# Optimization experiments

Hardware: AMD Instinct MI355X
Metric: run time of the kernel (lower is better)

Reference implementation:

```python
import jax, jax.numpy as jnp
import numpy as np

N_HEADS = 8
N_GROUPS = 32
EPS = 1e-5


def setup_inputs() -> dict:
    key = jax.random.key(0)
    ks = jax.random.split(key, 3)
    B, C, H, W = 16, 512, 32, 32
    x = jax.random.normal(ks[0], (B, C, H, W), dtype=jnp.float32)
    gn_w = jnp.ones((C,), dtype=jnp.float32)
    gn_b = jnp.zeros((C,), dtype=jnp.float32)
    qkv_w = jax.random.normal(ks[1], (3 * C, C), dtype=jnp.float32) * (1.0 / np.sqrt(C))
    qkv_b = jnp.zeros((3 * C,), dtype=jnp.float32)
    proj_w = jax.random.normal(ks[2], (C, C), dtype=jnp.float32) * (1.0 / np.sqrt(C))
    proj_b = jnp.zeros((C,), dtype=jnp.float32)
    return {"x": x, "gn_w": gn_w, "gn_b": gn_b, "qkv_w": qkv_w,
            "qkv_b": qkv_b, "proj_w": proj_w, "proj_b": proj_b}


def reference(x, gn_w, gn_b, qkv_w, qkv_b, proj_w, proj_b):
    b, c, h, w = x.shape
    t = h * w
    xf = x.reshape(b, c, t)                       # [B, C, T]

    # GroupNorm(32, C): normalize over (C//G, T) per group, then per-channel affine
    xg = xf.reshape(b, N_GROUPS, -1)              # [B, G, (C//G)*T]
    mean = xg.mean(axis=-1, keepdims=True)
    var = xg.var(axis=-1, keepdims=True)
    xn = ((xg - mean) * jax.lax.rsqrt(var + EPS)).reshape(b, c, t)
    xn = xn * gn_w[:, None] + gn_b[:, None]

    # 1x1 conv = channel GEMM -> qkv [B, 3C, T]
    qkv = jnp.einsum('oc,bct->bot', qkv_w, xn) + qkv_b[:, None]

    # legacy head split: reshape BEFORE splitting q,k,v
    qkv = qkv.reshape(b * N_HEADS, 3 * c // N_HEADS, t)
    ch = qkv.shape[1] // 3                        # = C // n_heads
    q, k, v = jnp.split(qkv, 3, axis=1)
    scale = 1.0 / np.sqrt(np.sqrt(ch))
    weight = jnp.einsum('bct,bcs->bts', q * scale, k * scale)
    weight = jax.nn.softmax(weight.astype(jnp.float32), axis=-1).astype(weight.dtype)
    a = jnp.einsum('bts,bcs->bct', weight, v)     # [B*H, ch, T]

    hh = a.reshape(b, c, t)
    hh = jnp.einsum('oc,bct->bot', proj_w, hh) + proj_b[:, None]
    return (xf + hh).reshape(b, c, h, w)
```

## Files before the change

kernel.cpp:

```cpp
#include <hip/hip_runtime.h>
#include <hip/hip_bf16.h>
#include <stdint.h>

#define B_ 16
#define C_ 512
#define T_ 1024
#define NH_ 8

typedef __attribute__((ext_vector_type(8))) short bf16x8;
typedef __attribute__((ext_vector_type(4))) float f32x4;
typedef __attribute__((ext_vector_type(16))) float f32x16;
typedef __attribute__((ext_vector_type(4))) unsigned short us4;
typedef __attribute__((ext_vector_type(4))) uint32_t u32x4;
typedef __attribute__((ext_vector_type(2))) uint32_t u32x2;

__device__ __forceinline__ unsigned short f2bf(float f) {
  union { float f; uint32_t u; } v; v.f = f;
  uint32_t r = v.u + 0x7FFFu + ((v.u >> 16) & 1u);
  return (unsigned short)(r >> 16);
}

__device__ __forceinline__ uint32_t cvtpk_bf16(float lo, float hi) {
  uint32_t r;
  asm("v_cvt_pk_bf16_f32 %0, %1, %2" : "=v"(r) : "v"(lo), "v"(hi));
  return r;
}

__device__ __forceinline__ f32x4 mfma_bf16(bf16x8 a, bf16x8 b, f32x4 c) {
  asm("v_mfma_f32_16x16x32_bf16 %0, %1, %2, %0" : "+v"(c) : "v"(a), "v"(b));
  return c;
}

__device__ __forceinline__ f32x16 mfma32_bf16(bf16x8 a, bf16x8 b, f32x16 c) {
  asm("v_mfma_f32_32x32x16_bf16 %0, %1, %2, %0" : "+v"(c) : "v"(a), "v"(b));
  return c;
}

__device__ __forceinline__ void swap32(uint32_t& a, uint32_t& b) {
  asm("v_permlane32_swap_b32 %0, %1" : "+v"(a), "+v"(b));
}

typedef const __attribute__((address_space(1))) uint32_t* gas1_t;
typedef __attribute__((address_space(3))) uint32_t* las3_t;

__device__ __forceinline__ void async16(const void* g, void* lds) {
  __builtin_amdgcn_global_load_lds((gas1_t)(uintptr_t)g,
                                   (las3_t)(uint32_t)(uintptr_t)lds, 16, 0, 0);
}

#define SCLF 0.18033688011112044f

__global__ __launch_bounds__(256) void convert_w_kernel(
    const float* __restrict__ qkv_w, const float* __restrict__ proj_w,
    unsigned short* __restrict__ wq, unsigned short* __restrict__ wp) {
  int i = blockIdx.x * 256 + threadIdx.x;
  const float4* src;
  unsigned short* dst;
  int rel = i;
  if (i < 196608) { src = (const float4*)qkv_w; dst = wq; }
  else            { src = (const float4*)proj_w; dst = wp; rel = i - 196608; }
  float4 v = src[rel];
  us4 o;
  o.x = f2bf(v.x); o.y = f2bf(v.y); o.z = f2bf(v.z); o.w = f2bf(v.w);
  *(us4*)&dst[(size_t)rel * 4] = o;
}

__global__ __launch_bounds__(256) void groupnorm_kernel(
    const float* __restrict__ x, const float* __restrict__ gn_w,
    const float* __restrict__ gn_b, unsigned short* __restrict__ xnT) {
  const int blk = blockIdx.x;
  const int b = blk >> 5, g = blk & 31;
  const int tid = threadIdx.x;
  const float4* x4 = (const float4*)(x + (((size_t)(b * C_ + g * 16)) << 10));

  float4 v[16];
  float s1 = 0.f, s2 = 0.f;
#pragma unroll
  for (int i = 0; i < 16; ++i) {
    v[i] = x4[tid + i * 256];
    s1 += v[i].x + v[i].y + v[i].z + v[i].w;
    s2 += v[i].x * v[i].x + v[i].y * v[i].y + v[i].z * v[i].z + v[i].w * v[i].w;
  }
#pragma unroll
  for (int m = 32; m; m >>= 1) { s1 += __shfl_xor(s1, m); s2 += __shfl_xor(s2, m); }

  __shared__ float r1[4], r2[4], stats[2];
  const int wv = tid >> 6;
  if ((tid & 63) == 0) { r1[wv] = s1; r2[wv] = s2; }
  __syncthreads();
  if (tid == 0) {
    float a = r1[0] + r1[1] + r1[2] + r1[3];
    float q = r2[0] + r2[1] + r2[2] + r2[3];
    float mean = a * (1.f / 16384.f);
    float var = q * (1.f / 16384.f) - mean * mean;
    stats[0] = mean;
    stats[1] = rsqrtf(var + 1e-5f);
  }
  __syncthreads();
  const float mean = stats[0], rsig = stats[1];

  float wc[16], bc[16];
#pragma unroll
  for (int c = 0; c < 16; ++c) {
    const float w0 = gn_w[g * 16 + c] * rsig;
    wc[c] = w0;
    bc[c] = gn_b[g * 16 + c] - mean * w0;
  }
#pragma unroll
  for (int r = 0; r < 4; ++r) {
    uint32_t o[8];
#pragma unroll
    for (int c2 = 0; c2 < 8; ++c2) {
      const float a = ((const float*)&v[2 * c2])[r] * wc[2 * c2] + bc[2 * c2];
      const float q = ((const float*)&v[2 * c2 + 1])[r] * wc[2 * c2 + 1] + bc[2 * c2 + 1];
      o[c2] = cvtpk_bf16(a, q);
    }
    unsigned short* dst = &xnT[(((size_t)(b * T_ + tid * 4 + r)) << 9) + g * 16];
    u32x4 lo; lo.x = o[0]; lo.y = o[1]; lo.z = o[2]; lo.w = o[3];
    u32x4 hi; hi.x = o[4]; hi.y = o[5]; hi.z = o[6]; hi.w = o[7];
    *(u32x4*)dst = lo;
    *(u32x4*)(dst + 8) = hi;
  }
}

template <int MODE>
__global__ __launch_bounds__(256) void gemm_nt_kernel(
    const unsigned short* __restrict__ A, const unsigned short* __restrict__ Bw,
    const float* __restrict__ bias, unsigned short* __restrict__ qfb,
    unsigned short* __restrict__ kfb, unsigned short* __restrict__ vfb,
    const float* __restrict__ xres, float* __restrict__ out) {
  const int b = blockIdx.z;
  const int m0 = blockIdx.y * 128;
  const int n0 = blockIdx.x * 128;
  const int tid = threadIdx.x;
  const int w = tid >> 6, ln = tid & 63;
  const int r15 = ln & 15, r4 = ln >> 4;

  __shared__ __attribute__((aligned(16))) char smem[40960];
  unsigned short* As = (unsigned short*)smem;
  unsigned short* Bs = (unsigned short*)(smem + 16384);

  const unsigned short* Ab = A + (((size_t)(b * T_ + m0)) << 9);
  const unsigned short* Bb = Bw + ((size_t)n0 << 9);

  f32x4 acc[4][4] = {};
  const int wm = (w >> 1) << 6, wn = (w & 1) << 6;

  for (int kt = 0; kt < 8; ++kt) {
    const int k0 = kt << 6;
    __syncthreads();
#pragma unroll
    for (int j = 0; j < 4; ++j) {
      const int slot = (j << 6) + ln;
      const int row = slot >> 3;
      const int chg = (slot & 7) ^ (row & 7);
      async16(Ab + (((size_t)(w * 32 + row)) << 9) + k0 + chg * 8,
              (char*)As + w * 4096 + j * 1024);
      async16(Bb + (((size_t)(w * 32 + row)) << 9) + k0 + chg * 8,
              (char*)Bs + w * 4096 + j * 1024);
    }
    __syncthreads();
#pragma unroll
    for (int kk = 0; kk < 2; ++kk) {
      bf16x8 af[4], bfr[4];
#pragma unroll
      for (int i = 0; i < 4; ++i) {
        const int ra = wm + i * 16 + r15;
        const int ch = r4 + kk * 4;
        af[i] = *(const bf16x8*)((const char*)As + ra * 128 + ((ch ^ (ra & 7)) << 4));
        const int rb = wn + i * 16 + r15;
        bfr[i] = *(const bf16x8*)((const char*)Bs + rb * 128 + ((ch ^ (rb & 7)) << 4));
      }
#pragma unroll
      for (int i = 0; i < 4; ++i)
#pragma unroll
        for (int j = 0; j < 4; ++j)
          acc[i][j] = mfma_bf16(af[i], bfr[j], acc[i][j]);
    }
  }

  if constexpr (MODE == 0) {
    __syncthreads();
    const int seg = w & 1;
    const int typ3 = (n0 >> 7) % 3;
    int st;
    if (typ3 == 0) st = seg;
    else if (typ3 == 1) st = seg ? 0 : 2;
    else st = seg ? 2 : 1;
    const int hseg = (n0 + seg * 64) / 192;
    char* segp = smem + seg * 20480;
    const int q5 = ln & 31, hi = ln >> 5;

    if (st < 2) {
      unsigned short* qkL = (unsigned short*)segp;
      const float scl = (st == 0) ? SCLF : 1.f;
#pragma unroll
      for (int j = 0; j < 4; ++j) {
        const int c = j * 16 + r15;
        const float bsv = bias[n0 + seg * 64 + c];
#pragma unroll
        for (int i = 0; i < 4; ++i) {
          const int t0 = wm + i * 16 + r4 * 4;
#pragma unroll
          for (int r = 0; r < 4; ++r)
            qkL[(t0 + r) * 80 + c] = f2bf((acc[i][j][r] + bsv) * scl);
        }
      }
      __syncthreads();
      unsigned short* dst = (st == 0) ? qfb : kfb;
      const size_t hb = ((size_t)(b * NH_ + hseg)) << 16;
#pragma unroll
      for (int u = 0; u < 8; ++u) {
        const int qbl = (w >> 1) * 2 + (u >> 2);
        const int ks = u & 3;
        bf16x8 val = *(const bf16x8*)&qkL[(qbl * 32 + q5) * 80 + ks * 16 + hi * 8];
        *(bf16x8*)&dst[hb + ((((m0 >> 5) + qbl) * 4 + ks) * 64 + ln) * 8] = val;
      }
    } else {
      unsigned short* vL = (unsigned short*)segp;
#pragma unroll
      for (int j = 0; j < 4; ++j) {
        const int c = j * 16 + r15;
        const float bsv = bias[n0 + seg * 64 + c];
#pragma unroll
        for (int i = 0; i < 4; ++i) {
          const int t0 = wm + i * 16 + r4 * 4;
          u32x2 pk;
          pk.x = cvtpk_bf16(acc[i][j][0] + bsv, acc[i][j][1] + bsv);
          pk.y = cvtpk_bf16(acc[i][j][2] + bsv, acc[i][j][3] + bsv);
          *(u32x2*)&vL[c * 144 + t0] = pk;
        }
      }
      __syncthreads();
      const size_t hb = ((size_t)(b * NH_ + hseg)) << 16;
      const int ktl = w >> 1;
#pragma unroll
      for (int u = 0; u < 8; ++u) {
        const int ks = u >> 1, cb = u & 1;
        bf16x8 val = *(const bf16x8*)&vL[(cb * 32 + q5) * 144 +
                                         ktl * 64 + ks * 16 + hi * 8];
        *(bf16x8*)&vfb[hb + ((((m0 >> 6) + ktl) * 8 + ks * 2 + cb) * 64 + ln) * 8] = val;
      }
    }
  } else {
#pragma unroll
    for (int i = 0; i < 4; ++i) {
      const int t = m0 + wm + i * 16 + r4 * 4;
#pragma unroll
      for (int j = 0; j < 4; ++j) {
        const int o = n0 + wn + j * 16 + r15;
        const float bsv = bias[o];
        const size_t base = (((size_t)(b * C_ + o)) << 10) + t;
        const float4 xr = *(const float4*)&xres[base];
        float4 ov;
        ov.x = acc[i][j][0] + bsv + xr.x;
        ov.y = acc[i][j][1] + bsv + xr.y;
        ov.z = acc[i][j][2] + bsv + xr.z;
        ov.w = acc[i][j][3] + bsv + xr.w;
        *(float4*)&out[base] = ov;
      }
    }
  }
}

__global__ __launch_bounds__(256) void attn_kernel(
    const unsigned short* __restrict__ Qf, const unsigned short* __restrict__ Kf,
    const unsigned short* __restrict__ Vf, unsigned short* __restrict__ aT) {
  const int lin = blockIdx.x;
  const int bh = (lin & 7) * 16 + (lin >> 5);
  const int qt = (lin >> 3) & 3;
  const int b = bh >> 3, h = bh & 7;
  const int tid = threadIdx.x;
  const int w = tid >> 6, ln = tid & 63;
  const int q5 = ln & 31, hi = ln >> 5;

  const unsigned short* qb_ = Qf + ((size_t)bh << 16);
  const unsigned short* kb = Kf + ((size_t)bh << 16);
  const unsigned short* vb = Vf + ((size_t)bh << 16);
  const int qw0 = qt * 8 + w * 2;

  bf16x8 qf[2][4];
#pragma unroll
  for (int qb = 0; qb < 2; ++qb)
#pragma unroll
    for (int ks = 0; ks < 4; ++ks)
      qf[qb][ks] = *(const bf16x8*)(qb_ + ((((qw0 + qb) * 4 + ks) * 64 + ln) << 3));

  float l_run[2] = {0.f, 0.f};
  f32x16 acc[2][2] = {};

  for (int t = 0; t < 16; ++t) {
    bf16x8 kf[2][4], vf[2][4];
#pragma unroll
    for (int k2 = 0; k2 < 2; ++k2)
#pragma unroll
      for (int ks = 0; ks < 4; ++ks)
        kf[k2][ks] = *(const bf16x8*)(kb + ((((t * 2 + k2) * 4 + ks) * 64 + ln) << 3));
#pragma unroll
    for (int cb = 0; cb < 2; ++cb)
#pragma unroll
      for (int ks = 0; ks < 4; ++ks)
        vf[cb][ks] = *(const bf16x8*)(vb + (((t * 8 + ks * 2 + cb) * 64 + ln) << 3));

    f32x16 s[2][2] = {};
    __builtin_amdgcn_s_setprio(1);
#pragma unroll
    for (int qb = 0; qb < 2; ++qb)
#pragma unroll
      for (int k2 = 0; k2 < 2; ++k2)
#pragma unroll
        for (int ks = 0; ks < 4; ++ks)
          s[qb][k2] = mfma32_bf16(kf[k2][ks], qf[qb][ks], s[qb][k2]);
    __builtin_amdgcn_s_setprio(0);

#pragma unroll
    for (int qb = 0; qb < 2; ++qb) {
      float pe[32];
#pragma unroll
      for (int u = 0; u < 16; ++u)
        pe[u] = __builtin_amdgcn_exp2f(fminf(s[qb][0][u], 60.f));
#pragma unroll
      for (int u = 0; u < 16; ++u)
        pe[16 + u] = __builtin_amdgcn_exp2f(fminf(s[qb][1][u], 60.f));

      float sm[16];
#pragma unroll
      for (int m = 0; m < 16; ++m) sm[m] = pe[2 * m] + pe[2 * m + 1];
#pragma unroll
      for (int d = 8; d; d >>= 1)
#pragma unroll
        for (int m = 0; m < 8; ++m)
          if (m < d) sm[m] += sm[m + d];
      l_run[qb] += sm[0];

      bf16x8 pf[4];
#pragma unroll
      for (int ks = 0; ks < 4; ++ks) {
        const float* ps = pe + ks * 8;
        uint32_t Aw = cvtpk_bf16(ps[0], ps[1]);
        uint32_t Bw2 = cvtpk_bf16(ps[2], ps[3]);
        uint32_t Cw = cvtpk_bf16(ps[4], ps[5]);
        uint32_t Dw = cvtpk_bf16(ps[6], ps[7]);
        swap32(Aw, Cw);
        swap32(Bw2, Dw);
        union { uint32_t u[4]; bf16x8 v; } cv;
        cv.u[0] = Aw; cv.u[1] = Bw2; cv.u[2] = Cw; cv.u[3] = Dw;
        pf[ks] = cv.v;
      }

      __builtin_amdgcn_s_setprio(1);
#pragma unroll
      for (int cb = 0; cb < 2; ++cb)
#pragma unroll
        for (int ks = 0; ks < 4; ++ks)
          acc[qb][cb] = mfma32_bf16(vf[cb][ks], pf[ks], acc[qb][cb]);
      __builtin_amdgcn_s_setprio(0);
    }
  }

#pragma unroll
  for (int qb = 0; qb < 2; ++qb) {
    const float l = l_run[qb] + __shfl_xor(l_run[qb], 32);
    const float inv = 1.f / l;
    const size_t rowb = ((size_t)(b * T_ + (qw0 + qb) * 32 + q5)) << 9;
#pragma unroll
    for (int cb = 0; cb < 2; ++cb)
#pragma unroll
      for (int m = 0; m < 4; ++m) {
        u32x2 o;
        o.x = cvtpk_bf16(acc[qb][cb][4 * m] * inv, acc[qb][cb][4 * m + 1] * inv);
        o.y = cvtpk_bf16(acc[qb][cb][4 * m + 2] * inv, acc[qb][cb][4 * m + 3] * inv);
        *(u32x2*)&aT[rowb + h * 64 + cb * 32 + 8 * m + 4 * hi] = o;
      }
  }
}

extern "C" void kernel_launch(void* const* d_in, const int* in_sizes, int n_in,
                              void* d_out, int out_size, void* d_ws, size_t ws_size,
                              hipStream_t stream) {
  (void)in_sizes; (void)n_in; (void)out_size; (void)ws_size;
  const float* x      = (const float*)d_in[0];
  const float* gn_w   = (const float*)d_in[1];
  const float* gn_b   = (const float*)d_in[2];
  const float* qkv_w  = (const float*)d_in[3];
  const float* qkv_b  = (const float*)d_in[4];
  const float* proj_w = (const float*)d_in[5];
  const float* proj_b = (const float*)d_in[6];
  float* out = (float*)d_out;

  char* ws = (char*)d_ws;
  unsigned short* wq  = (unsigned short*)(ws);
  unsigned short* wp  = (unsigned short*)(ws + 1572864);
  unsigned short* xnT = (unsigned short*)(ws + 2097152);
  unsigned short* Qf  = (unsigned short*)(ws + 18874368);
  unsigned short* Kf  = (unsigned short*)(ws + 35651584);
  unsigned short* Vf  = (unsigned short*)(ws + 52428800);

  convert_w_kernel<<<1024, 256, 0, stream>>>(qkv_w, proj_w, wq, wp);
  groupnorm_kernel<<<512, 256, 0, stream>>>(x, gn_w, gn_b, xnT);
  gemm_nt_kernel<0><<<dim3(12, 8, 16), 256, 0, stream>>>(xnT, wq, qkv_b, Qf, Kf, Vf,
                                                         nullptr, nullptr);
  attn_kernel<<<512, 256, 0, stream>>>(Qf, Kf, Vf, xnT );
  gemm_nt_kernel<1><<<dim3(4, 8, 16), 256, 0, stream>>>(xnT, wp, proj_b, nullptr,
                                                        nullptr, nullptr, x, out);
}
```

Measured before the change: 129.0 us.

## Double-buffer K/V tiles in LDS via async loads in attention kernel

The attention kernel now stages each K and V tile into shared memory with asynchronous global-to-LDS copies. Two buffers let the next tile be prefetched while the current one is computed, and workgroup barriers sit around each iteration. Previously each wave read K/V fragments straight from global memory, and all four waves loaded the same data. The change also drops the fminf clamp before exp2, which removes some VALU work but can overflow if scores grow large. The extra barriers and LDS use may reduce occupancy.

```diff
diff --git a/kernel.cpp b/kernel.cpp
--- a/kernel.cpp
+++ b/kernel.cpp
@@ -274,11 +274,22 @@
   const int w = tid >> 6, ln = tid & 63;
   const int q5 = ln & 31, hi = ln >> 5;
 
+  __shared__ __attribute__((aligned(16))) unsigned short Ks[2][4096];
+  __shared__ __attribute__((aligned(16))) unsigned short Vs[2][4096];
+
   const unsigned short* qb_ = Qf + ((size_t)bh << 16);
   const unsigned short* kb = Kf + ((size_t)bh << 16);
   const unsigned short* vb = Vf + ((size_t)bh << 16);
   const int qw0 = qt * 8 + w * 2;
 
+  const unsigned short* sgb = (w < 2) ? kb : vb;
+  const int shalf = (w & 1) * 2048;
+
+#pragma unroll
+  for (int j = 0; j < 4; ++j)
+    async16(sgb + shalf + j * 512 + ln * 8,
+            (char*)(w < 2 ? Ks[0] : Vs[0]) + (w & 1) * 4096 + j * 1024);
+
   bf16x8 qf[2][4];
 #pragma unroll
   for (int qb = 0; qb < 2; ++qb)
@@ -290,17 +301,36 @@
   f32x16 acc[2][2] = {};
 
   for (int t = 0; t < 16; ++t) {
+    const int p = t & 1;
+    if (t < 15) {
+      const int nt = (t + 1) * 4096;
+#pragma unroll
+      for (int j = 0; j < 4; ++j)
+        async16(sgb + nt + shalf + j * 512 + ln * 8,
+                (char*)(w < 2 ? Ks[p ^ 1] : Vs[p ^ 1]) + (w & 1) * 4096 + j * 1024);
+      __builtin_amdgcn_sched_barrier(0);
+      asm volatile("s_waitcnt vmcnt(4)" ::: "memory");
+    } else {
+      __builtin_amdgcn_sched_barrier(0);
+      asm volatile("s_waitcnt vmcnt(0)" ::: "memory");
+    }
+    __builtin_amdgcn_s_barrier();
+    asm volatile("" ::: "memory");
+    __builtin_amdgcn_sched_barrier(0);
+
     bf16x8 kf[2][4], vf[2][4];
 #pragma unroll
     for (int k2 = 0; k2 < 2; ++k2)
 #pragma unroll
       for (int ks = 0; ks < 4; ++ks)
-        kf[k2][ks] = *(const bf16x8*)(kb + ((((t * 2 + k2) * 4 + ks) * 64 + ln) << 3));
+        kf[k2][ks] = *(const bf16x8*)((const char*)Ks[p] +
+                                      (((k2 * 4 + ks) << 10) + ln * 16));
 #pragma unroll
     for (int cb = 0; cb < 2; ++cb)
 #pragma unroll
       for (int ks = 0; ks < 4; ++ks)
-        vf[cb][ks] = *(const bf16x8*)(vb + (((t * 8 + ks * 2 + cb) * 64 + ln) << 3));
+        vf[cb][ks] = *(const bf16x8*)((const char*)Vs[p] +
+                                      (((ks * 2 + cb) << 10) + ln * 16));
 
     f32x16 s[2][2] = {};
     __builtin_amdgcn_s_setprio(1);
@@ -318,10 +348,10 @@
       float pe[32];
 #pragma unroll
       for (int u = 0; u < 16; ++u)
-        pe[u] = __builtin_amdgcn_exp2f(fminf(s[qb][0][u], 60.f));
+        pe[u] = __builtin_amdgcn_exp2f(s[qb][0][u]);
 #pragma unroll
       for (int u = 0; u < 16; ++u)
-        pe[16 + u] = __builtin_amdgcn_exp2f(fminf(s[qb][1][u], 60.f));
+        pe[16 + u] = __builtin_amdgcn_exp2f(s[qb][1][u]);
 
       float sm[16];
 #pragma unroll
@@ -356,6 +386,10 @@
           acc[qb][cb] = mfma32_bf16(vf[cb][ks], pf[ks], acc[qb][cb]);
       __builtin_amdgcn_s_setprio(0);
     }
+
+    __builtin_amdgcn_sched_barrier(0);
+    __builtin_amdgcn_s_barrier();
+    asm volatile("" ::: "memory");
   }
 
 #pragma unroll
```

Measured after the change: 124.0 us. 1.04x faster.
